# Performance work log

Measured on AMD Instinct MI355X. Metric: run time of the kernel, lower is better.

## Reference

```python
import jax, jax.numpy as jnp
import numpy as np
from jax import lax

INT8_NARROW = (-127.0, 127.0)   # brevitas Int8WeightPerTensorFloat (narrow range)
INT8_FULL = (-128.0, 127.0)     # brevitas Int8ActPerTensorFloat
INT32 = (-2.0**31, 2.0**31 - 1)


def _fake_quant(v, scale, qmin, qmax):
    # round-to-nearest, clip, dequant (per-tensor)
    return jnp.clip(jnp.round(v / scale), qmin, qmax) * scale


def _conv(x, w, stride):
    return lax.conv_general_dilated(
        x, w, window_strides=(stride, stride), padding=[(1, 1), (1, 1)],
        dimension_numbers=("NCHW", "OIHW", "NCHW"))


def setup_inputs() -> dict:
    key = jax.random.key(0)
    ks = jax.random.split(key, 5)
    B, Cin, Cout, H = 64, 256, 512, 28
    x = jax.random.normal(ks[0], (B, Cin, H, H), dtype=jnp.float32)
    w1 = jax.random.normal(ks[1], (Cout, Cin, 3, 3), dtype=jnp.float32) * 0.05
    b1 = jax.random.normal(ks[2], (Cout,), dtype=jnp.float32) * 0.01
    w2 = jax.random.normal(ks[3], (Cout, Cout, 3, 3), dtype=jnp.float32) * 0.05
    b2 = jax.random.normal(ks[4], (Cout,), dtype=jnp.float32) * 0.01
    return {
        "x": x, "w1": w1, "b1": b1, "w2": w2, "b2": b2,
        "in_scale": jnp.full((1,), 0.05, dtype=jnp.float32),
        "act1_scale": jnp.full((1,), 0.05, dtype=jnp.float32),
        "act2_scale": jnp.full((1,), 0.05, dtype=jnp.float32),
    }


def reference(x, w1, b1, w2, b2, in_scale, act1_scale, act2_scale):
    s_in = in_scale[0]
    s_a1 = act1_scale[0]
    s_a2 = act2_scale[0]

    # conv1: per-tensor int8 weight fake-quant (max-abs stats, narrow range)
    s_w1 = jnp.max(jnp.abs(w1)) / 127.0
    wq1 = _fake_quant(w1, s_w1, *INT8_NARROW)
    bq1 = _fake_quant(b1, s_in * s_w1, *INT32)  # Int32Bias: scale = in_scale*w_scale
    out = _conv(x, wq1, 2) + bq1[None, :, None, None]

    # act1: int8 activation fake-quant (learned per-tensor scale)
    out = _fake_quant(out, s_a1, *INT8_FULL)

    # conv2
    s_w2 = jnp.max(jnp.abs(w2)) / 127.0
    wq2 = _fake_quant(w2, s_w2, *INT8_NARROW)
    bq2 = _fake_quant(b2, s_a1 * s_w2, *INT32)
    out = _conv(out, wq2, 1) + bq2[None, :, None, None]

    # act2
    out = _fake_quant(out, s_a2, *INT8_FULL)
    return out
```

## Files before the change

### kernel.cpp

```cpp
#include <hip/hip_runtime.h>

typedef int i32x4 __attribute__((ext_vector_type(4)));

__device__ __forceinline__ void gl_lds16(const signed char* g, signed char* l) {
    __builtin_amdgcn_global_load_lds(
        (const __attribute__((address_space(1))) void*)g,
        (__attribute__((address_space(3))) void*)l, 16, 0, 0);
}

#define XQ_SCALE 2048.0f
#define XQ_DELTA (1.0f / 2048.0f)

__global__ void init_ws_kernel(unsigned* p) {
    if (threadIdx.x < 2) p[threadIdx.x] = 0u;
}

__global__ void absmax2_kernel(const float* __restrict__ w1, const float* __restrict__ w2,
                               unsigned* __restrict__ out) {
    const bool second = blockIdx.x >= 256;
    const float* w = second ? w2 : w1;
    const int n4 = second ? (512 * 512 * 9 / 4) : (512 * 256 * 9 / 4);
    unsigned* o = out + (second ? 1 : 0);
    float m = 0.0f;
    for (int i = (blockIdx.x & 255) * 256 + threadIdx.x; i < n4; i += 65536) {
        float4 v = ((const float4*)w)[i];
        m = fmaxf(m, fmaxf(fmaxf(fabsf(v.x), fabsf(v.y)), fmaxf(fabsf(v.z), fabsf(v.w))));
    }
#pragma unroll
    for (int off = 32; off > 0; off >>= 1)
        m = fmaxf(m, __shfl_down(m, off));
    if ((threadIdx.x & 63) == 0)
        atomicMax(o, __float_as_uint(m));
}

__global__ __launch_bounds__(256) void prep_all_kernel(
    const float* __restrict__ x,
    const float* __restrict__ w1, const float* __restrict__ w2,
    const float* __restrict__ b1, const float* __restrict__ b2,
    const unsigned* __restrict__ absbits,
    const float* __restrict__ in_scale, const float* __restrict__ act1_scale,
    signed char* __restrict__ wq1, signed char* __restrict__ wq2,
    float* __restrict__ bq1, float* __restrict__ bq2,
    signed char* __restrict__ xhi, signed char* __restrict__ xlo,
    signed char* __restrict__ act) {
    __shared__ __align__(16) signed char sw[4608];
    __shared__ float t[128][33];
    const int blk = blockIdx.x;
    const int tid = threadIdx.x;
    const uint4 z = {0, 0, 0, 0};

    if (blk < 512) {
        const int n = blk;
        const float inv_s = 127.0f / __uint_as_float(absbits[0]);
#pragma unroll
        for (int rd = 0; rd < 9; ++rd) {
            const int idx = rd * 256 + tid;
            const float v = w1[n * 2304 + idx];
            float q = rintf(v * inv_s);
            q = fminf(fmaxf(q, -127.0f), 127.0f);
            const int cin = idx / 9;
            const int r = idx - cin * 9;
            sw[r * 256 + cin] = (signed char)(int)q;
        }
        __syncthreads();
        if (tid < 144) *(uint4*)&wq1[n * 2304 + tid * 16] = *(const uint4*)&sw[tid * 16];
    } else if (blk < 1024) {
        const int n = blk - 512;
        const float inv_s = 127.0f / __uint_as_float(absbits[1]);
#pragma unroll
        for (int rd = 0; rd < 18; ++rd) {
            const int idx = rd * 256 + tid;
            const float v = w2[n * 4608 + idx];
            float q = rintf(v * inv_s);
            q = fminf(fmaxf(q, -127.0f), 127.0f);
            const int cin = idx / 9;
            const int r = idx - cin * 9;
            sw[r * 512 + cin] = (signed char)(int)q;
        }
        __syncthreads();
        for (int o = tid; o < 288; o += 256)
            *(uint4*)&wq2[n * 4608 + o * 16] = *(const uint4*)&sw[o * 16];
    } else if (blk == 1024) {
        for (int idx = tid; idx < 1024; idx += 256) {
            if (idx < 512) {
                const float s = (*in_scale) * (__uint_as_float(absbits[0]) * (1.0f / 127.0f));
                float q = rintf(b1[idx] / s);
                q = fminf(fmaxf(q, -2147483648.0f), 2147483648.0f);
                bq1[idx] = q * s;
            } else {
                const int j = idx - 512;
                const float s = (*act1_scale) * (__uint_as_float(absbits[1]) * (1.0f / 127.0f));
                float q = rintf(b2[j] / s);
                q = fminf(fmaxf(q, -2147483648.0f), 2147483648.0f);
                bq2[j] = q * s;
            }
        }
    } else if (blk < 1489) {
        const int thr = (blk - 1025) * 256 + tid;
        const int b = thr / (116 * 16);
        const int rr = thr - b * (116 * 16);
        const int p = rr >> 4;
        const int ch = rr & 15;
        int h, w;
        if (p < 30)      { h = 0;          w = p; }
        else if (p < 60) { h = 29;         w = p - 30; }
        else if (p < 88) { h = p - 60 + 1; w = 0; }
        else             { h = p - 88 + 1; w = 29; }
        const int off = (b * 900 + h * 30 + w) * 256 + ch * 16;
        *(uint4*)(xhi + off) = z;
        *(uint4*)(xlo + off) = z;
    } else if (blk < 1969) {
        const int thr = (blk - 1489) * 256 + tid;
        const int b = thr / (60 * 32);
        const int rr = thr - b * (60 * 32);
        const int p = rr >> 5;
        const int ch = rr & 31;
        int h, w;
        if (p < 16)      { h = 0;          w = p; }
        else if (p < 32) { h = 15;         w = p - 16; }
        else if (p < 46) { h = p - 32 + 1; w = 0; }
        else             { h = p - 46 + 1; w = 15; }
        const int off = (b * 256 + h * 16 + w) * 512 + ch * 16;
        *(uint4*)(act + off) = z;
    } else {
        const int xb = blk - 1969;
        const int hwb = xb % 25;
        const int rest = xb / 25;
        const int cb = rest & 1;
        const int b = rest >> 1;
        const int c0 = cb * 128;
        const int hw0 = hwb * 32;
#pragma unroll
        for (int ci = 0; ci < 16; ++ci) {
            const int crow = (tid >> 5) + ci * 8;
            const int hw = hw0 + (tid & 31);
            float v = 0.0f;
            if (hw < 784) v = x[(b * 256 + c0 + crow) * 784 + hw];
            t[crow][tid & 31] = v;
        }
        __syncthreads();
        const int hw_l = tid >> 3;
        const int cg = (tid & 7) * 16;
        const int hw = hw0 + hw_l;
        if (hw < 784) {
            union { signed char c[16]; uint4 u; } ph, pl;
#pragma unroll
            for (int j = 0; j < 16; ++j) {
                const float v = t[cg + j][hw_l];
                int q = (int)rintf(v * XQ_SCALE);
                q = max(-16383, min(16383, q));
                ph.c[j] = (signed char)(q >> 7);
                pl.c[j] = (signed char)(q & 127);
            }
            const int r = hw / 28;
            const int o = (b * 900 + (r + 1) * 30 + (hw - r * 28) + 1) * 256 + c0 + cg;
            *(uint4*)&xhi[o] = ph.u;
            *(uint4*)&xlo[o] = pl.u;
        }
    }
}

template<int CIN, int STRIDE, int HP, int HOUT, bool SPLIT, bool FINAL>
__global__ __launch_bounds__(256) void conv_gemm_kernel(
    const signed char* __restrict__ Ahi,
    const signed char* __restrict__ Alo,
    const signed char* __restrict__ Wt,
    const float* __restrict__ bias,
    const unsigned* __restrict__ wabs,
    const float* __restrict__ s_pre,
    const float* __restrict__ s_act,
    signed char* __restrict__ act_out,
    float* __restrict__ out_final)
{
    constexpr int K = 9 * CIN;
    constexpr int HW = HOUT * HOUT;
    constexpr int NIT = K / 64;
    constexpr int NC = SPLIT ? 6 : 4;
    constexpr int NACC = SPLIT ? 8 : 4;
    constexpr int BUFSZ = SPLIT ? 24576 : 16384;
    constexpr int BSOFF = SPLIT ? 16384 : 8192;

    __shared__ __align__(16) signed char smem[2][BUFSZ];

    const int tid = threadIdx.x;
    const int lane = tid & 63;
    const int wv = tid >> 6;
    const int wm = wv & 1;
    const int wn = wv >> 1;
    const int quad = lane >> 4;
    const int l16 = lane & 15;
    const int m0 = blockIdx.y * 128;
    const int n0 = blockIdx.x * 128;

    const int lrow = lane >> 2;
    const int lslot = lane & 3;

    const signed char* srcb[NC];
    int dsto[NC];
    bool isA[NC];
#pragma unroll
    for (int i = 0; i < NC; ++i) {
        const int g = wv * NC + i;
        int type, c;
        if (SPLIT) {
            type = (g < 8) ? 0 : (g < 16 ? 1 : 2);
            c = (g < 8) ? g : (g < 16 ? g - 8 : g - 16);
        } else {
            type = (g < 8) ? 0 : 2;
            c = (g < 8) ? g : g - 8;
        }
        const int r = c * 16 + lrow;
        const int koff = (lslot ^ ((r >> 1) & 3)) * 16;
        if (type == 2) {
            srcb[i] = Wt + (n0 + r) * K + koff;
            dsto[i] = BSOFF + c * 1024;
            isA[i] = false;
        } else {
            const int m = m0 + r;
            const int b = m / HW;
            const int rem = m - b * HW;
            const int oh = rem / HOUT;
            const int ow = rem - oh * HOUT;
            const int off = ((b * HP + oh * STRIDE) * HP + ow * STRIDE) * CIN + koff;
            srcb[i] = (type == 0 ? Ahi : Alo) + off;
            dsto[i] = (type == 0 ? 0 : 8192) + c * 1024;
            isA[i] = true;
        }
    }

    i32x4 acc[NACC][4];
#pragma unroll
    for (int mi = 0; mi < NACC; ++mi)
#pragma unroll
        for (int ni = 0; ni < 4; ++ni)
            acc[mi][ni] = i32x4{0, 0, 0, 0};

    {
        constexpr int ashift0 = 0;
#pragma unroll
        for (int i = 0; i < NC; ++i)
            gl_lds16(srcb[i] + (isA[i] ? ashift0 : 0), &smem[0][dsto[i]]);
    }

    int p = 0;
    for (int it = 0; it < NIT; ++it) {
        __syncthreads();
        if (it + 1 < NIT) {
            const int k0 = (it + 1) * 64;
            const int r9 = k0 / CIN;
            const int kh = r9 / 3;
            const int kw = r9 - kh * 3;
            const int ashift = (kh * HP + kw) * CIN + (k0 & (CIN - 1));
            const int q2 = p ^ 1;
#pragma unroll
            for (int i = 0; i < NC; ++i)
                gl_lds16(srcb[i] + (isA[i] ? ashift : k0), &smem[q2][dsto[i]]);
        }

        i32x4 af[NACC];
        i32x4 bfr[4];
#pragma unroll
        for (int mi = 0; mi < 4; ++mi) {
            const int row = wm * 64 + mi * 16 + l16;
            const int sl = (quad ^ ((row >> 1) & 3)) * 16;
            af[mi] = *(const i32x4*)&smem[p][row * 64 + sl];
            if constexpr (SPLIT)
                af[mi + 4] = *(const i32x4*)&smem[p][8192 + row * 64 + sl];
        }
#pragma unroll
        for (int ni = 0; ni < 4; ++ni) {
            const int row = wn * 64 + ni * 16 + l16;
            const int sl = (quad ^ ((row >> 1) & 3)) * 16;
            bfr[ni] = *(const i32x4*)&smem[p][BSOFF + row * 64 + sl];
        }
#pragma unroll
        for (int mi = 0; mi < 4; ++mi)
#pragma unroll
            for (int ni = 0; ni < 4; ++ni) {
                acc[mi][ni] = __builtin_amdgcn_mfma_i32_16x16x64_i8(af[mi], bfr[ni], acc[mi][ni], 0, 0, 0);
                if constexpr (SPLIT)
                    acc[mi + 4][ni] = __builtin_amdgcn_mfma_i32_16x16x64_i8(af[mi + 4], bfr[ni], acc[mi + 4][ni], 0, 0, 0);
            }
        p ^= 1;
    }

    float alpha = __uint_as_float(*wabs) * (1.0f / 127.0f);
    if (FINAL) alpha *= *s_pre;
    if (SPLIT) alpha *= XQ_DELTA;
    const float sact = *s_act;

    float bv[4];
#pragma unroll
    for (int ni = 0; ni < 4; ++ni)
        bv[ni] = bias[n0 + wn * 64 + ni * 16 + l16];

#pragma unroll
    for (int mi = 0; mi < 4; ++mi) {
#pragma unroll
        for (int i = 0; i < 4; ++i) {
            const int m = m0 + wm * 64 + mi * 16 + quad * 4 + i;
            const int b = m / HW;
            const int rem = m - b * HW;
            const int oh = rem / HOUT;
            const int ow = rem - oh * HOUT;
#pragma unroll
            for (int ni = 0; ni < 4; ++ni) {
                const int col = n0 + wn * 64 + ni * 16 + l16;
                int tot = acc[mi][ni][i];
                if constexpr (SPLIT) tot = tot * 128 + acc[mi + 4][ni][i];
                const float v = (float)tot * alpha + bv[ni];
                float q = rintf(v / sact);
                q = fminf(fmaxf(q, -128.0f), 127.0f);
                if (FINAL) {
                    out_final[(b * 512 + col) * HW + oh * HOUT + ow] = q * sact;
                } else {
                    act_out[(b * 256 + (oh + 1) * 16 + (ow + 1)) * 512 + col] = (signed char)(int)q;
                }
            }
        }
    }
}

extern "C" void kernel_launch(void* const* d_in, const int* in_sizes, int n_in,
                              void* d_out, int out_size, void* d_ws, size_t ws_size,
                              hipStream_t stream) {
    const float* x  = (const float*)d_in[0];
    const float* w1 = (const float*)d_in[1];
    const float* b1 = (const float*)d_in[2];
    const float* w2 = (const float*)d_in[3];
    const float* b2 = (const float*)d_in[4];
    const float* in_scale   = (const float*)d_in[5];
    const float* act1_scale = (const float*)d_in[6];
    const float* act2_scale = (const float*)d_in[7];
    float* out = (float*)d_out;

    char* ws = (char*)d_ws;
    unsigned* absbits = (unsigned*)(ws + 0);
    float* bq1 = (float*)(ws + 64);
    float* bq2 = (float*)(ws + 2112);
    signed char* wq1 = (signed char*)(ws + 8192);
    signed char* wq2 = (signed char*)(ws + 1187840);
    signed char* xhi = (signed char*)(ws + 3547136);
    signed char* xlo = (signed char*)(ws + 18292736);
    signed char* act = (signed char*)(ws + 33038336);

    init_ws_kernel<<<1, 64, 0, stream>>>(absbits);
    absmax2_kernel<<<512, 256, 0, stream>>>(w1, w2, absbits);

    prep_all_kernel<<<5169, 256, 0, stream>>>(
        x, w1, w2, b1, b2, absbits, in_scale, act1_scale,
        wq1, wq2, bq1, bq2, xhi, xlo, act);

    conv_gemm_kernel<256, 2, 30, 14, true, false><<<dim3(4, 98), 256, 0, stream>>>(
        xhi, xlo, wq1, bq1, absbits, act1_scale, act1_scale, act, nullptr);

    conv_gemm_kernel<512, 1, 16, 14, false, true><<<dim3(4, 98), 256, 0, stream>>>(
        act, nullptr, wq2, bq2, absbits + 1, act1_scale, act2_scale, nullptr, out);
}
```

Baseline: 263.7 us.

## Retile conv GEMMs to 64x128 with 128-wide K stages and drop atomic absmax

The conv GEMM kernels move from 256-thread 128x128 tiles with 64-wide K steps to 128-thread 64x128 tiles with 128-wide K steps. This doubles the grid and halves the number of barriers per K. The loop is unrolled two stages at a time with a new XOR swizzle. The weight abs-max now writes per-block partials that each prep block reduces itself, which removes the init kernel and the atomics. This costs some redundant partial reductions and more LDS per block.

```diff
diff --git a/kernel.cpp b/kernel.cpp
--- a/kernel.cpp
+++ b/kernel.cpp
@@ -11,16 +11,13 @@
 #define XQ_SCALE 2048.0f
 #define XQ_DELTA (1.0f / 2048.0f)
 
-__global__ void init_ws_kernel(unsigned* p) {
-    if (threadIdx.x < 2) p[threadIdx.x] = 0u;
-}
-
-__global__ void absmax2_kernel(const float* __restrict__ w1, const float* __restrict__ w2,
-                               unsigned* __restrict__ out) {
+__global__ __launch_bounds__(256) void absmax2_kernel(const float* __restrict__ w1,
+                                                      const float* __restrict__ w2,
+                                                      float* __restrict__ part) {
+    __shared__ float sred[4];
     const bool second = blockIdx.x >= 256;
     const float* w = second ? w2 : w1;
-    const int n4 = second ? (512 * 512 * 9 / 4) : (512 * 256 * 9 / 4);
-    unsigned* o = out + (second ? 1 : 0);
+    const int n4 = second ? 589824 : 294912;
     float m = 0.0f;
     for (int i = (blockIdx.x & 255) * 256 + threadIdx.x; i < n4; i += 65536) {
         float4 v = ((const float4*)w)[i];
@@ -29,29 +26,45 @@
 #pragma unroll
     for (int off = 32; off > 0; off >>= 1)
         m = fmaxf(m, __shfl_down(m, off));
-    if ((threadIdx.x & 63) == 0)
-        atomicMax(o, __float_as_uint(m));
+    if ((threadIdx.x & 63) == 0) sred[threadIdx.x >> 6] = m;
+    __syncthreads();
+    if (threadIdx.x == 0)
+        part[blockIdx.x] = fmaxf(fmaxf(sred[0], sred[1]), fmaxf(sred[2], sred[3]));
+}
+
+__device__ __forceinline__ float block_max256(const float* __restrict__ part, int base,
+                                              float* __restrict__ sred) {
+    float m = part[base + (threadIdx.x & 255)];
+#pragma unroll
+    for (int off = 32; off > 0; off >>= 1)
+        m = fmaxf(m, __shfl_down(m, off));
+    __syncthreads();
+    if ((threadIdx.x & 63) == 0) sred[threadIdx.x >> 6] = m;
+    __syncthreads();
+    return fmaxf(fmaxf(sred[0], sred[1]), fmaxf(sred[2], sred[3]));
 }
 
 __global__ __launch_bounds__(256) void prep_all_kernel(
     const float* __restrict__ x,
     const float* __restrict__ w1, const float* __restrict__ w2,
     const float* __restrict__ b1, const float* __restrict__ b2,
-    const unsigned* __restrict__ absbits,
+    const float* __restrict__ part,
     const float* __restrict__ in_scale, const float* __restrict__ act1_scale,
     signed char* __restrict__ wq1, signed char* __restrict__ wq2,
     float* __restrict__ bq1, float* __restrict__ bq2,
+    float* __restrict__ wmax,
     signed char* __restrict__ xhi, signed char* __restrict__ xlo,
     signed char* __restrict__ act) {
     __shared__ __align__(16) signed char sw[4608];
     __shared__ float t[128][33];
+    __shared__ float sred[4];
     const int blk = blockIdx.x;
     const int tid = threadIdx.x;
     const uint4 z = {0, 0, 0, 0};
 
     if (blk < 512) {
+        const float inv_s = 127.0f / block_max256(part, 0, sred);
         const int n = blk;
-        const float inv_s = 127.0f / __uint_as_float(absbits[0]);
 #pragma unroll
         for (int rd = 0; rd < 9; ++rd) {
             const int idx = rd * 256 + tid;
@@ -65,8 +78,8 @@
         __syncthreads();
         if (tid < 144) *(uint4*)&wq1[n * 2304 + tid * 16] = *(const uint4*)&sw[tid * 16];
     } else if (blk < 1024) {
+        const float inv_s = 127.0f / block_max256(part, 256, sred);
         const int n = blk - 512;
-        const float inv_s = 127.0f / __uint_as_float(absbits[1]);
 #pragma unroll
         for (int rd = 0; rd < 18; ++rd) {
             const int idx = rd * 256 + tid;
@@ -81,15 +94,21 @@
         for (int o = tid; o < 288; o += 256)
             *(uint4*)&wq2[n * 4608 + o * 16] = *(const uint4*)&sw[o * 16];
     } else if (blk == 1024) {
+        const float m1 = block_max256(part, 0, sred);
+        const float m2 = block_max256(part, 256, sred);
+        if (tid == 0) { wmax[0] = m1; wmax[1] = m2; }
+        if (tid < 512) {
+            const float s = (*in_scale) * (m1 * (1.0f / 127.0f));
+        }
         for (int idx = tid; idx < 1024; idx += 256) {
             if (idx < 512) {
-                const float s = (*in_scale) * (__uint_as_float(absbits[0]) * (1.0f / 127.0f));
+                const float s = (*in_scale) * (m1 * (1.0f / 127.0f));
                 float q = rintf(b1[idx] / s);
                 q = fminf(fmaxf(q, -2147483648.0f), 2147483648.0f);
                 bq1[idx] = q * s;
             } else {
                 const int j = idx - 512;
-                const float s = (*act1_scale) * (__uint_as_float(absbits[1]) * (1.0f / 127.0f));
+                const float s = (*act1_scale) * (m2 * (1.0f / 127.0f));
                 float q = rintf(b2[j] / s);
                 q = fminf(fmaxf(q, -2147483648.0f), 2147483648.0f);
                 bq2[j] = q * s;
@@ -161,12 +180,12 @@
 }
 
 template<int CIN, int STRIDE, int HP, int HOUT, bool SPLIT, bool FINAL>
-__global__ __launch_bounds__(256) void conv_gemm_kernel(
+__global__ __launch_bounds__(128) void conv_gemm_kernel(
     const signed char* __restrict__ Ahi,
     const signed char* __restrict__ Alo,
     const signed char* __restrict__ Wt,
     const float* __restrict__ bias,
-    const unsigned* __restrict__ wabs,
+    const float* __restrict__ wmax,
     const float* __restrict__ s_pre,
     const float* __restrict__ s_act,
     signed char* __restrict__ act_out,
@@ -174,26 +193,25 @@
 {
     constexpr int K = 9 * CIN;
     constexpr int HW = HOUT * HOUT;
-    constexpr int NIT = K / 64;
-    constexpr int NC = SPLIT ? 6 : 4;
+    constexpr int NIT = K / 128;
+    constexpr int NC = SPLIT ? 16 : 12;
     constexpr int NACC = SPLIT ? 8 : 4;
-    constexpr int BUFSZ = SPLIT ? 24576 : 16384;
     constexpr int BSOFF = SPLIT ? 16384 : 8192;
-
-    __shared__ __align__(16) signed char smem[2][BUFSZ];
+    constexpr int BUFSZ = BSOFF + 16384;
+
+    __shared__ __align__(16) signed char sm0[BUFSZ];
+    __shared__ __align__(16) signed char sm1[BUFSZ];
 
     const int tid = threadIdx.x;
     const int lane = tid & 63;
     const int wv = tid >> 6;
-    const int wm = wv & 1;
-    const int wn = wv >> 1;
     const int quad = lane >> 4;
     const int l16 = lane & 15;
-    const int m0 = blockIdx.y * 128;
+    const int m0 = blockIdx.y * 64;
     const int n0 = blockIdx.x * 128;
 
-    const int lrow = lane >> 2;
-    const int lslot = lane & 3;
+    const int lrow = lane >> 3;
+    const int koff = ((lane & 7) ^ lrow) * 16;
 
     const signed char* srcb[NC];
     int dsto[NC];
@@ -209,8 +227,7 @@
             type = (g < 8) ? 0 : 2;
             c = (g < 8) ? g : g - 8;
         }
-        const int r = c * 16 + lrow;
-        const int koff = (lslot ^ ((r >> 1) & 3)) * 16;
+        const int r = c * 8 + lrow;
         if (type == 2) {
             srcb[i] = Wt + (n0 + r) * K + koff;
             dsto[i] = BSOFF + c * 1024;
@@ -235,56 +252,57 @@
         for (int ni = 0; ni < 4; ++ni)
             acc[mi][ni] = i32x4{0, 0, 0, 0};
 
-    {
-        constexpr int ashift0 = 0;
+    auto stage = [&](int k0, signed char* buf) {
+        const int r9 = k0 / CIN;
+        const int kh = r9 / 3;
+        const int kw = r9 - kh * 3;
+        const int ashift = (kh * HP + kw) * CIN + (k0 & (CIN - 1));
 #pragma unroll
         for (int i = 0; i < NC; ++i)
-            gl_lds16(srcb[i] + (isA[i] ? ashift0 : 0), &smem[0][dsto[i]]);
-    }
-
-    int p = 0;
-    for (int it = 0; it < NIT; ++it) {
-        __syncthreads();
-        if (it + 1 < NIT) {
-            const int k0 = (it + 1) * 64;
-            const int r9 = k0 / CIN;
-            const int kh = r9 / 3;
-            const int kw = r9 - kh * 3;
-            const int ashift = (kh * HP + kw) * CIN + (k0 & (CIN - 1));
-            const int q2 = p ^ 1;
-#pragma unroll
-            for (int i = 0; i < NC; ++i)
-                gl_lds16(srcb[i] + (isA[i] ? ashift : k0), &smem[q2][dsto[i]]);
-        }
-
-        i32x4 af[NACC];
-        i32x4 bfr[4];
-#pragma unroll
-        for (int mi = 0; mi < 4; ++mi) {
-            const int row = wm * 64 + mi * 16 + l16;
-            const int sl = (quad ^ ((row >> 1) & 3)) * 16;
-            af[mi] = *(const i32x4*)&smem[p][row * 64 + sl];
-            if constexpr (SPLIT)
-                af[mi + 4] = *(const i32x4*)&smem[p][8192 + row * 64 + sl];
-        }
-#pragma unroll
-        for (int ni = 0; ni < 4; ++ni) {
-            const int row = wn * 64 + ni * 16 + l16;
-            const int sl = (quad ^ ((row >> 1) & 3)) * 16;
-            bfr[ni] = *(const i32x4*)&smem[p][BSOFF + row * 64 + sl];
-        }
-#pragma unroll
-        for (int mi = 0; mi < 4; ++mi)
+            gl_lds16(srcb[i] + (isA[i] ? ashift : k0), buf + dsto[i]);
+    };
+
+    auto compute = [&](const signed char* buf) {
+#pragma unroll
+        for (int ks = 0; ks < 2; ++ks) {
+            i32x4 af[NACC];
+            i32x4 bfr[4];
+#pragma unroll
+            for (int mi = 0; mi < 4; ++mi) {
+                const int row = mi * 16 + l16;
+                const int sl = ((ks * 4 + quad) ^ (row & 7)) * 16;
+                af[mi] = *(const i32x4*)&buf[row * 128 + sl];
+                if constexpr (SPLIT)
+                    af[mi + 4] = *(const i32x4*)&buf[8192 + row * 128 + sl];
+            }
 #pragma unroll
             for (int ni = 0; ni < 4; ++ni) {
-                acc[mi][ni] = __builtin_amdgcn_mfma_i32_16x16x64_i8(af[mi], bfr[ni], acc[mi][ni], 0, 0, 0);
-                if constexpr (SPLIT)
-                    acc[mi + 4][ni] = __builtin_amdgcn_mfma_i32_16x16x64_i8(af[mi + 4], bfr[ni], acc[mi + 4][ni], 0, 0, 0);
-            }
-        p ^= 1;
-    }
-
-    float alpha = __uint_as_float(*wabs) * (1.0f / 127.0f);
+                const int row = wv * 64 + ni * 16 + l16;
+                const int sl = ((ks * 4 + quad) ^ (row & 7)) * 16;
+                bfr[ni] = *(const i32x4*)&buf[BSOFF + row * 128 + sl];
+            }
+#pragma unroll
+            for (int mi = 0; mi < 4; ++mi)
+#pragma unroll
+                for (int ni = 0; ni < 4; ++ni) {
+                    acc[mi][ni] = __builtin_amdgcn_mfma_i32_16x16x64_i8(af[mi], bfr[ni], acc[mi][ni], 0, 0, 0);
+                    if constexpr (SPLIT)
+                        acc[mi + 4][ni] = __builtin_amdgcn_mfma_i32_16x16x64_i8(af[mi + 4], bfr[ni], acc[mi + 4][ni], 0, 0, 0);
+                }
+        }
+    };
+
+    stage(0, sm0);
+    for (int it = 0; it < NIT; it += 2) {
+        __syncthreads();
+        stage((it + 1) * 128, sm1);
+        compute(sm0);
+        __syncthreads();
+        if (it + 2 < NIT) stage((it + 2) * 128, sm0);
+        compute(sm1);
+    }
+
+    float alpha = (*wmax) * (1.0f / 127.0f);
     if (FINAL) alpha *= *s_pre;
     if (SPLIT) alpha *= XQ_DELTA;
     const float sact = *s_act;
@@ -292,20 +310,20 @@
     float bv[4];
 #pragma unroll
     for (int ni = 0; ni < 4; ++ni)
-        bv[ni] = bias[n0 + wn * 64 + ni * 16 + l16];
+        bv[ni] = bias[n0 + wv * 64 + ni * 16 + l16];
 
 #pragma unroll
     for (int mi = 0; mi < 4; ++mi) {
 #pragma unroll
         for (int i = 0; i < 4; ++i) {
-            const int m = m0 + wm * 64 + mi * 16 + quad * 4 + i;
+            const int m = m0 + mi * 16 + quad * 4 + i;
             const int b = m / HW;
             const int rem = m - b * HW;
             const int oh = rem / HOUT;
             const int ow = rem - oh * HOUT;
 #pragma unroll
             for (int ni = 0; ni < 4; ++ni) {
-                const int col = n0 + wn * 64 + ni * 16 + l16;
+                const int col = n0 + wv * 64 + ni * 16 + l16;
                 int tot = acc[mi][ni][i];
                 if constexpr (SPLIT) tot = tot * 128 + acc[mi + 4][ni][i];
                 const float v = (float)tot * alpha + bv[ni];
@@ -335,25 +353,25 @@
     float* out = (float*)d_out;
 
     char* ws = (char*)d_ws;
-    unsigned* absbits = (unsigned*)(ws + 0);
-    float* bq1 = (float*)(ws + 64);
-    float* bq2 = (float*)(ws + 2112);
+    float* part = (float*)(ws + 0);
+    float* wmax = (float*)(ws + 2048);
+    float* bq1 = (float*)(ws + 2176);
+    float* bq2 = (float*)(ws + 4224);
     signed char* wq1 = (signed char*)(ws + 8192);
     signed char* wq2 = (signed char*)(ws + 1187840);
     signed char* xhi = (signed char*)(ws + 3547136);
     signed char* xlo = (signed char*)(ws + 18292736);
     signed char* act = (signed char*)(ws + 33038336);
 
-    init_ws_kernel<<<1, 64, 0, stream>>>(absbits);
-    absmax2_kernel<<<512, 256, 0, stream>>>(w1, w2, absbits);
+    absmax2_kernel<<<512, 256, 0, stream>>>(w1, w2, part);
 
     prep_all_kernel<<<5169, 256, 0, stream>>>(
-        x, w1, w2, b1, b2, absbits, in_scale, act1_scale,
-        wq1, wq2, bq1, bq2, xhi, xlo, act);
-
-    conv_gemm_kernel<256, 2, 30, 14, true, false><<<dim3(4, 98), 256, 0, stream>>>(
-        xhi, xlo, wq1, bq1, absbits, act1_scale, act1_scale, act, nullptr);
-
-    conv_gemm_kernel<512, 1, 16, 14, false, true><<<dim3(4, 98), 256, 0, stream>>>(
-        act, nullptr, wq2, bq2, absbits + 1, act1_scale, act2_scale, nullptr, out);
-}
+        x, w1, w2, b1, b2, part, in_scale, act1_scale,
+        wq1, wq2, bq1, bq2, wmax, xhi, xlo, act);
+
+    conv_gemm_kernel<256, 2, 30, 14, true, false><<<dim3(4, 196), 128, 0, stream>>>(
+        xhi, xlo, wq1, bq1, wmax, act1_scale, act1_scale, act, nullptr);
+
+    conv_gemm_kernel<512, 1, 16, 14, false, true><<<dim3(4, 196), 128, 0, stream>>>(
+        act, nullptr, wq2, bq2, wmax + 1, act1_scale, act2_scale, nullptr, out);
+}
```

New measurement: 256.2 us. 2.8% less time.
